# Optimization experiments

Hardware: AMD Instinct MI355X
Metric: run time of the kernel (lower is better)

## Reference

```python
import jax, jax.numpy as jnp
import numpy as np

EMBED_DIM = 1024
NUM_HEADS = 16
HEAD_DIM = EMBED_DIM // NUM_HEADS


def setup_inputs() -> dict:
    key = jax.random.key(0)
    ks = jax.random.split(key, 7)
    B, S, D = 2, 2048, EMBED_DIM
    scale = 1.0 / np.sqrt(D)
    return {
        "query": jax.random.normal(ks[0], (B, S, D), dtype=jnp.float32),
        "key": jax.random.normal(ks[1], (B, S, D), dtype=jnp.float32),
        "value": jax.random.normal(ks[2], (B, S, D), dtype=jnp.float32),
        "W_qkv": jax.random.normal(ks[3], (D, 3 * D), dtype=jnp.float32) * scale,
        "b_qkv": jnp.zeros((3 * D,), dtype=jnp.float32),
        "W_out": jax.random.normal(ks[4], (D, D), dtype=jnp.float32) * scale,
        "b_out": jnp.zeros((D,), dtype=jnp.float32),
    }


def reference(query, key, value, W_qkv, b_qkv, W_out, b_out):
    # NOTE: the original torch forward ignores `key` and `value` — q,k,v all
    # come from qkv_proj(query). We keep them as args for signature fidelity.
    B, S, D = query.shape
    H, hd = NUM_HEADS, HEAD_DIM
    scale = hd ** -0.5

    qkv = query @ W_qkv + b_qkv                      # [B, S, 3D]
    qkv = qkv.reshape(B, S, 3, H, hd)
    q = jnp.transpose(qkv[:, :, 0], (0, 2, 1, 3))    # [B, H, S, hd]
    k = jnp.transpose(qkv[:, :, 1], (0, 2, 1, 3))
    v = jnp.transpose(qkv[:, :, 2], (0, 2, 1, 3))

    scores = jnp.einsum("bhsd,bhtd->bhst", q, k) * scale  # [B, H, S, S]
    attn = jax.nn.softmax(scores, axis=-1)
    out = jnp.einsum("bhst,bhtd->bhsd", attn, v)           # [B, H, S, hd]
    out = jnp.transpose(out, (0, 2, 1, 3)).reshape(B, S, D)
    return out @ W_out + b_out
```

## Files before the change

### kernel.cpp

```cpp
#include <hip/hip_runtime.h>
#include <stdint.h>

#define DEV static __device__ __forceinline__

typedef __attribute__((ext_vector_type(4))) float f32x4;
typedef __attribute__((ext_vector_type(16))) float f32x16;
typedef __attribute__((ext_vector_type(8))) short bf16x8;
typedef bf16x8 __attribute__((may_alias)) bf16x8_a;
typedef __attribute__((ext_vector_type(2))) unsigned int u32x2;
typedef u32x2 __attribute__((may_alias)) u32x2_a;

DEV unsigned short f2bf(float f) {
  union { float f; unsigned int u; } v; v.f = f;
  return (unsigned short)((v.u + 0x7FFFu + ((v.u >> 16) & 1u)) >> 16);
}

DEV float bf2f(unsigned short s) {
  union { unsigned int u; float f; } v; v.u = ((unsigned int)s) << 16;
  return v.f;
}

DEV float fast_exp2(float x) {
  float r;
  asm("v_exp_f32 %0, %1" : "=v"(r) : "v"(x));
  return r;
}

DEV unsigned int pktrunc(float lo, float hi) {
  union { float f; unsigned int u; } a, b; a.f = lo; b.f = hi;
  return __builtin_amdgcn_perm(b.u, a.u, 0x07060302u);
}

DEV void gload_lds16(const void* g, void* l) {
  __builtin_amdgcn_global_load_lds(
      (const __attribute__((address_space(1))) unsigned int*)g,
      (__attribute__((address_space(3))) unsigned int*)l, 16, 0, 0);
}

DEV void transpose_body(const float* __restrict__ in, unsigned short* __restrict__ out,
                        int R, int C, int bx, int by, int t, float (*tile)[33]) {
  const int r = t >> 3, c4 = (t & 7) << 2;
  const int tr = by << 5, tc = bx << 5;
  const float4 v = *(const float4*)(in + (size_t)(tr + r) * C + tc + c4);
  tile[r][c4] = v.x; tile[r][c4 + 1] = v.y; tile[r][c4 + 2] = v.z; tile[r][c4 + 3] = v.w;
  __syncthreads();
  ushort4 o;
  o.x = f2bf(tile[c4][r]); o.y = f2bf(tile[c4 + 1][r]);
  o.z = f2bf(tile[c4 + 2][r]); o.w = f2bf(tile[c4 + 3][r]);
  *(ushort4*)(out + (size_t)(tc + r) * R + tr + c4) = o;
}

__global__ __launch_bounds__(256) void prep_k(const float4* __restrict__ q4,
                                              ushort4* __restrict__ Xb,
                                              const float* __restrict__ Wqkv,
                                              unsigned short* __restrict__ WqkvT,
                                              const float* __restrict__ Wout,
                                              unsigned short* __restrict__ WoutT) {
  __shared__ float tile[32][33];
  const int t = threadIdx.x, bid = blockIdx.x;
  if (bid < 4096) {
    const int i = bid * 256 + t;
    float4 f = q4[i];
    ushort4 o; o.x = f2bf(f.x); o.y = f2bf(f.y); o.z = f2bf(f.z); o.w = f2bf(f.w);
    Xb[i] = o;
  } else if (bid < 4096 + 3072) {
    const int id = bid - 4096;
    transpose_body(Wqkv, WqkvT, 1024, 3072, id % 96, id / 96, t, tile);
  } else {
    const int id = bid - 4096 - 3072;
    transpose_body(Wout, WoutT, 1024, 1024, id & 31, id >> 5, t, tile);
  }
}

template <int EPI, int BN>
__global__ __launch_bounds__(256, 3) void gemm_bt(const unsigned short* __restrict__ A,
                                                  const unsigned short* __restrict__ BT,
                                                  const float* __restrict__ bias,
                                                  float* __restrict__ Cout,
                                                  unsigned short* __restrict__ q_buf,
                                                  unsigned short* __restrict__ k_buf,
                                                  unsigned short* __restrict__ vT_buf,
                                                  int M, int N, int K) {
  constexpr int NI = BN / 32;
  constexpr int NW = BN / 2;
  __shared__ unsigned short As[128 * 64];
  __shared__ unsigned short Bs[BN * 64];
  const int t = threadIdx.x, w = t >> 6, l = t & 63;
  const int wm = w >> 1, wn = w & 1;
  const int lg = l >> 4, ln = l & 15;

  const int xcd = blockIdx.x & 7, jb = blockIdx.x >> 3;
  const int m0 = (xcd * 4 + (jb & 3)) * 128;
  const int n0 = (jb >> 2) * BN;

  const int sch = (t & 7) ^ ((t >> 3) & 7);

  f32x4 acc[4][NI] = {};

#define STAGE97(k0)                                                                      \
  do {                                                                                   \
    _Pragma("unroll")                                                                    \
    for (int j = 0; j < 4; ++j)                                                          \
      gload_lds16(A + (size_t)(m0 + (t >> 3) + j * 32) * K + (k0) + sch * 8,             \
                  &As[((t >> 3) + j * 32) * 64 + (t & 7) * 8]);                          \
    _Pragma("unroll")                                                                    \
    for (int j = 0; j < BN / 32; ++j)                                                    \
      gload_lds16(BT + (size_t)(n0 + (t >> 3) + j * 32) * K + (k0) + sch * 8,            \
                  &Bs[((t >> 3) + j * 32) * 64 + (t & 7) * 8]);                          \
  } while (0)

  for (int kt = 0; kt < K; kt += 64) {
    STAGE97(kt);
    __syncthreads();
#pragma unroll
    for (int kk = 0; kk < 2; ++kk) {
      bf16x8 af[4], bfr[NI];
#pragma unroll
      for (int mi = 0; mi < 4; ++mi)
        af[mi] = *(const bf16x8_a*)&As[(wm * 64 + mi * 16 + ln) * 64 +
                                       (((kk * 4 + lg) ^ (ln & 7)) << 3)];
#pragma unroll
      for (int ni = 0; ni < NI; ++ni)
        bfr[ni] = *(const bf16x8_a*)&Bs[(wn * NW + ni * 16 + ln) * 64 +
                                        (((kk * 4 + lg) ^ (ln & 7)) << 3)];
#pragma unroll
      for (int mi = 0; mi < 4; ++mi)
#pragma unroll
        for (int ni = 0; ni < NI; ++ni)
          acc[mi][ni] = __builtin_amdgcn_mfma_f32_16x16x32_bf16(af[mi], bfr[ni], acc[mi][ni], 0, 0, 0);
    }
    __syncthreads();
  }
#undef STAGE97

#pragma unroll
  for (int ni = 0; ni < NI; ++ni) {
    const int c = n0 + wn * NW + ni * 16 + ln;
    const float bv = bias[c];
    if (EPI == 1) {
      const int which = c >> 10;
      const int h = (c >> 6) & 15;
      const int d = c & 63;
#pragma unroll
      for (int mi = 0; mi < 4; ++mi) {
        const int mrow = m0 + wm * 64 + mi * 16 + lg * 4;
        const int b = mrow >> 11, s = mrow & 2047;
        const size_t bh = (size_t)(b * 16 + h);
        f32x4 v = acc[mi][ni];
        if (which == 0) {
          const float QSCALE = 0.125f * 1.44269504088896340736f;
          unsigned short* dst = q_buf + (bh * 2048 + s) * 64 + d;
#pragma unroll
          for (int r = 0; r < 4; ++r) dst[(size_t)r * 64] = f2bf((v[r] + bv) * QSCALE);
        } else if (which == 1) {
          unsigned short* dst = k_buf + (bh * 2048 + s) * 64 + d;
#pragma unroll
          for (int r = 0; r < 4; ++r) dst[(size_t)r * 64] = f2bf(v[r] + bv);
        } else {
          const int sp = (s & ~12) | ((s & 4) << 1) | ((s & 8) >> 1);
          unsigned short* dst = vT_buf + (bh * 64 + d) * 2048 + sp;
          ushort4 o4;
          o4.x = f2bf(v[0] + bv); o4.y = f2bf(v[1] + bv); o4.z = f2bf(v[2] + bv); o4.w = f2bf(v[3] + bv);
          *(ushort4*)dst = o4;
        }
      }
    } else {
#pragma unroll
      for (int mi = 0; mi < 4; ++mi) {
        const int mrow = m0 + wm * 64 + mi * 16 + lg * 4;
        f32x4 v = acc[mi][ni];
#pragma unroll
        for (int r = 0; r < 4; ++r) Cout[(size_t)(mrow + r) * N + c] = v[r] + bv;
      }
    }
  }
}

template <int SPLIT>
__global__ __launch_bounds__(256, 4) void attn_k(const unsigned short* __restrict__ Qb,
                                                 const unsigned short* __restrict__ Kb,
                                                 const unsigned short* __restrict__ Vt,
                                                 unsigned short* __restrict__ AO,
                                                 unsigned short* __restrict__ Opart,
                                                 float* __restrict__ lpart) {
  constexpr int NT = 32 / SPLIT;
  const float SHIFT = -16.0f;
  __shared__ unsigned short Ks[2][64 * 64];
  __shared__ unsigned short Vs[2][64 * 64];

  const int t = threadIdx.x, w = t >> 6, l = t & 63;
  const int l31 = l & 31, lh = l >> 5;
  const int xcd = blockIdx.x & 7, idx = blockIdx.x >> 3;
  const int bh = xcd * 4 + (idx & 3);
  const int qt = (SPLIT == 2) ? ((idx >> 2) & 15) : (idx >> 2);
  const int half = (SPLIT == 2) ? (idx >> 6) : 0;
  const int b = bh >> 4, h = bh & 15;
  const unsigned short* Q = Qb + (size_t)bh * 2048 * 64;
  const unsigned short* K = Kb + (size_t)bh * 2048 * 64 + (size_t)half * NT * 64 * 64;
  const unsigned short* V = Vt + (size_t)bh * 64 * 2048 + half * NT * 64;
  const int qbase = qt * 128 + w * 32;

  const int srow = t >> 3;
  const int scol = ((t & 7) ^ (srow & 7)) << 3;
  const int dcol = (t & 7) << 3;

  bf16x8 qf[4];
#pragma unroll
  for (int kd = 0; kd < 4; ++kd)
    qf[kd] = *(const bf16x8_a*)(Q + (size_t)(qbase + l31) * 64 + kd * 16 + lh * 8);

  bf16x8 ones;
#pragma unroll
  for (int i = 0; i < 8; ++i) ones[i] = (short)0x3F80;

  f32x16 o32[2] = {};
  f32x16 lsum = {};

  {
    gload_lds16(K + (size_t)srow * 64 + scol,        &Ks[0][srow * 64 + dcol]);
    gload_lds16(K + (size_t)(srow + 32) * 64 + scol, &Ks[0][(srow + 32) * 64 + dcol]);
    gload_lds16(V + (size_t)srow * 2048 + scol,        &Vs[0][srow * 64 + dcol]);
    gload_lds16(V + (size_t)(srow + 32) * 2048 + scol, &Vs[0][(srow + 32) * 64 + dcol]);
  }
  __syncthreads();

  for (int tk = 0; tk < NT; ++tk) {
    const int cur = tk & 1;
    if (tk < NT - 1) {
      const int k1 = (tk + 1) * 64;
      const unsigned short* Kg = K + (size_t)k1 * 64;
      const unsigned short* Vg = V + k1;
      gload_lds16(Kg + (size_t)srow * 64 + scol,        &Ks[cur ^ 1][srow * 64 + dcol]);
      gload_lds16(Kg + (size_t)(srow + 32) * 64 + scol, &Ks[cur ^ 1][(srow + 32) * 64 + dcol]);
      gload_lds16(Vg + (size_t)srow * 2048 + scol,        &Vs[cur ^ 1][srow * 64 + dcol]);
      gload_lds16(Vg + (size_t)(srow + 32) * 2048 + scol, &Vs[cur ^ 1][(srow + 32) * 64 + dcol]);
    }

    f32x16 sa[2] = {};
#pragma unroll
    for (int m2 = 0; m2 < 2; ++m2)
#pragma unroll
      for (int kd = 0; kd < 4; ++kd) {
        const bf16x8 kf = *(const bf16x8_a*)
            &Ks[cur][(m2 * 32 + l31) * 64 + (((kd * 2 + lh) ^ (l & 7)) << 3)];
        sa[m2] = __builtin_amdgcn_mfma_f32_32x32x16_bf16(kf, qf[kd], sa[m2], 0, 0, 0);
      }

    bf16x8 vf0[4];
#pragma unroll
    for (int ksI = 0; ksI < 4; ++ksI)
      vf0[ksI] = *(const bf16x8_a*)&Vs[cur][l31 * 64 + (((ksI * 2 + lh) ^ (l & 7)) << 3)];

    unsigned int pk[2][8];
#pragma unroll
    for (int m2 = 0; m2 < 2; ++m2) {
      float p[16];
#pragma unroll
      for (int r = 0; r < 16; ++r) p[r] = fast_exp2(sa[m2][r] + SHIFT);
#pragma unroll
      for (int u = 0; u < 8; ++u) pk[m2][u] = pktrunc(p[2 * u], p[2 * u + 1]);
    }

    union { unsigned int u[4]; bf16x8 v; } pa[4];
#pragma unroll
    for (int m2 = 0; m2 < 2; ++m2)
#pragma unroll
      for (int ks2 = 0; ks2 < 2; ++ks2) {
        const int ksI = m2 * 2 + ks2;
        pa[ksI].u[0] = pk[m2][ks2 * 4 + 0];
        pa[ksI].u[1] = pk[m2][ks2 * 4 + 1];
        pa[ksI].u[2] = pk[m2][ks2 * 4 + 2];
        pa[ksI].u[3] = pk[m2][ks2 * 4 + 3];
      }
#pragma unroll
    for (int ksI = 0; ksI < 4; ++ksI) {
      const bf16x8 vf1 = *(const bf16x8_a*)
          &Vs[cur][(32 + l31) * 64 + (((ksI * 2 + lh) ^ (l & 7)) << 3)];
      o32[0] = __builtin_amdgcn_mfma_f32_32x32x16_bf16(pa[ksI].v, vf0[ksI], o32[0], 0, 0, 0);
      lsum   = __builtin_amdgcn_mfma_f32_32x32x16_bf16(pa[ksI].v, ones,     lsum,   0, 0, 0);
      o32[1] = __builtin_amdgcn_mfma_f32_32x32x16_bf16(pa[ksI].v, vf1,      o32[1], 0, 0, 0);
    }

    __syncthreads();
  }

  if (SPLIT == 2) {
    const size_t pbase = ((size_t)(half * 32 + bh) * 2048 + qbase);
#pragma unroll
    for (int nb = 0; nb < 2; ++nb)
#pragma unroll
      for (int r = 0; r < 16; ++r) {
        const int qrow = (r & 3) + 8 * (r >> 2) + 4 * lh;
        Opart[(pbase + qrow) * 64 + nb * 32 + l31] = f2bf(o32[nb][r]);
      }
    if (l31 == 0) {
#pragma unroll
      for (int r = 0; r < 16; ++r)
        lpart[pbase + (r & 3) + 8 * (r >> 2) + 4 * lh] = lsum[r];
    }
  } else {
#pragma unroll
    for (int nb = 0; nb < 2; ++nb)
#pragma unroll
      for (int r = 0; r < 16; ++r) {
        const int qrow = (r & 3) + 8 * (r >> 2) + 4 * lh;
        const size_t row = (size_t)b * 2048 + qbase + qrow;
        AO[row * 1024 + h * 64 + nb * 32 + l31] = f2bf(o32[nb][r] / lsum[r]);
      }
  }
}

__global__ __launch_bounds__(256) void merge_k(const unsigned short* __restrict__ Opart,
                                               const float* __restrict__ lpart,
                                               unsigned short* __restrict__ AO) {
  const int u = blockIdx.x * 256 + threadIdx.x;
  const int c8 = u & 7, s = (u >> 3) & 2047, bh = u >> 14;
  const int b = bh >> 4, h = bh & 15;
  const size_t r0 = (size_t)bh * 2048 + s;
  const size_t r1 = (size_t)(32 + bh) * 2048 + s;
  const bf16x8 a0 = *(const bf16x8_a*)(Opart + r0 * 64 + c8 * 8);
  const bf16x8 a1 = *(const bf16x8_a*)(Opart + r1 * 64 + c8 * 8);
  const float inv = 1.0f / (lpart[r0] + lpart[r1]);
  bf16x8 oo;
#pragma unroll
  for (int i = 0; i < 8; ++i)
    oo[i] = (short)f2bf((bf2f((unsigned short)a0[i]) + bf2f((unsigned short)a1[i])) * inv);
  *(bf16x8_a*)(AO + ((size_t)b * 2048 + s) * 1024 + h * 64 + c8 * 8) = oo;
}

extern "C" void kernel_launch(void* const* d_in, const int* in_sizes, int n_in,
                              void* d_out, int out_size, void* d_ws, size_t ws_size,
                              hipStream_t stream) {
  const float* query = (const float*)d_in[0];
  const float* W_qkv = (const float*)d_in[3];
  const float* b_qkv = (const float*)d_in[4];
  const float* W_out = (const float*)d_in[5];
  const float* b_out = (const float*)d_in[6];
  float* out = (float*)d_out;
  char* ws = (char*)d_ws;

  unsigned short* Xb    = (unsigned short*)(ws);
  unsigned short* WqkvT = (unsigned short*)(ws + 8388608);
  unsigned short* WoutT = (unsigned short*)(ws + 14680064);
  unsigned short* qb    = (unsigned short*)(ws + 16777216);
  unsigned short* kb    = (unsigned short*)(ws + 25165824);
  unsigned short* vT    = (unsigned short*)(ws + 33554432);
  unsigned short* Opart = (unsigned short*)(ws + 41943040);
  float*          lpart = (float*)(ws + 58720256);
  const bool split2 = ws_size >= 59244544;
  unsigned short* AO    = Xb;

  prep_k<<<8192, 256, 0, stream>>>((const float4*)query, (ushort4*)Xb,
                                   W_qkv, WqkvT, W_out, WoutT);
  gemm_bt<1, 128><<<768, 256, 0, stream>>>(Xb, WqkvT, b_qkv, nullptr, qb, kb, vT,
                                           4096, 3072, 1024);
  if (split2) {
    attn_k<2><<<1024, 256, 0, stream>>>(qb, kb, vT, nullptr, Opart, lpart);
    merge_k<<<2048, 256, 0, stream>>>(Opart, lpart, AO);
  } else {
    attn_k<1><<<512, 256, 0, stream>>>(qb, kb, vT, AO, nullptr, nullptr);
  }
  gemm_bt<0, 64><<<512, 256, 0, stream>>>(AO, WoutT, b_out, out, nullptr, nullptr, nullptr,
                                          4096, 1024, 1024);
}
```

Measured before the change: 113.8 us.

## Double per-wave query rows in attention to reuse K/V fragments

Each wave now handles 64 query rows (two 32-row blocks) instead of 32, so K and V fragments loaded from LDS are reused across two QK^T and PV passes. The block's query tile grows from 128 to 256 rows and the grid is halved, with launch bounds relaxed to 2 blocks per CU to give room for the doubled accumulators. The aim is fewer LDS reads and fewer global K/V tile loads per query row. The cost is higher register pressure, lower occupancy, and fewer blocks (512 in the split path) to fill the GPU.

```diff
diff --git a/kernel.cpp b/kernel.cpp
--- a/kernel.cpp
+++ b/kernel.cpp
@@ -177,7 +177,7 @@
 }
 
 template <int SPLIT>
-__global__ __launch_bounds__(256, 4) void attn_k(const unsigned short* __restrict__ Qb,
+__global__ __launch_bounds__(256, 2) void attn_k(const unsigned short* __restrict__ Qb,
                                                  const unsigned short* __restrict__ Kb,
                                                  const unsigned short* __restrict__ Vt,
                                                  unsigned short* __restrict__ AO,
@@ -192,29 +192,32 @@
   const int l31 = l & 31, lh = l >> 5;
   const int xcd = blockIdx.x & 7, idx = blockIdx.x >> 3;
   const int bh = xcd * 4 + (idx & 3);
-  const int qt = (SPLIT == 2) ? ((idx >> 2) & 15) : (idx >> 2);
-  const int half = (SPLIT == 2) ? (idx >> 6) : 0;
+  const int rest = idx >> 2;
+  const int qt = rest & 7;
+  const int half = (SPLIT == 2) ? (rest >> 3) : 0;
   const int b = bh >> 4, h = bh & 15;
   const unsigned short* Q = Qb + (size_t)bh * 2048 * 64;
   const unsigned short* K = Kb + (size_t)bh * 2048 * 64 + (size_t)half * NT * 64 * 64;
   const unsigned short* V = Vt + (size_t)bh * 64 * 2048 + half * NT * 64;
-  const int qbase = qt * 128 + w * 32;
+  const int qbase = qt * 256 + w * 64;
 
   const int srow = t >> 3;
   const int scol = ((t & 7) ^ (srow & 7)) << 3;
   const int dcol = (t & 7) << 3;
 
-  bf16x8 qf[4];
-#pragma unroll
-  for (int kd = 0; kd < 4; ++kd)
-    qf[kd] = *(const bf16x8_a*)(Q + (size_t)(qbase + l31) * 64 + kd * 16 + lh * 8);
+  bf16x8 qf[2][4];
+#pragma unroll
+  for (int qb = 0; qb < 2; ++qb)
+#pragma unroll
+    for (int kd = 0; kd < 4; ++kd)
+      qf[qb][kd] = *(const bf16x8_a*)(Q + (size_t)(qbase + qb * 32 + l31) * 64 + kd * 16 + lh * 8);
 
   bf16x8 ones;
 #pragma unroll
   for (int i = 0; i < 8; ++i) ones[i] = (short)0x3F80;
 
-  f32x16 o32[2] = {};
-  f32x16 lsum = {};
+  f32x16 o32[2][2] = {};
+  f32x16 lsum[2] = {};
 
   {
     gload_lds16(K + (size_t)srow * 64 + scol,        &Ks[0][srow * 64 + dcol]);
@@ -236,49 +239,57 @@
       gload_lds16(Vg + (size_t)(srow + 32) * 2048 + scol, &Vs[cur ^ 1][(srow + 32) * 64 + dcol]);
     }
 
-    f32x16 sa[2] = {};
+    bf16x8 kf[2][4];
 #pragma unroll
     for (int m2 = 0; m2 < 2; ++m2)
 #pragma unroll
-      for (int kd = 0; kd < 4; ++kd) {
-        const bf16x8 kf = *(const bf16x8_a*)
-            &Ks[cur][(m2 * 32 + l31) * 64 + (((kd * 2 + lh) ^ (l & 7)) << 3)];
-        sa[m2] = __builtin_amdgcn_mfma_f32_32x32x16_bf16(kf, qf[kd], sa[m2], 0, 0, 0);
+      for (int kd = 0; kd < 4; ++kd)
+        kf[m2][kd] = *(const bf16x8_a*)
+            &Ks[cur][(m2 * 32 + l31) * 64 + (((kd * 2 + lh) ^ (l31 & 7)) << 3)];
+    bf16x8 vf[2][4];
+#pragma unroll
+    for (int nb = 0; nb < 2; ++nb)
+#pragma unroll
+      for (int ksI = 0; ksI < 4; ++ksI)
+        vf[nb][ksI] = *(const bf16x8_a*)
+            &Vs[cur][(nb * 32 + l31) * 64 + (((ksI * 2 + lh) ^ (l31 & 7)) << 3)];
+
+#pragma unroll
+    for (int qb = 0; qb < 2; ++qb) {
+      f32x16 sa[2] = {};
+#pragma unroll
+      for (int m2 = 0; m2 < 2; ++m2)
+#pragma unroll
+        for (int kd = 0; kd < 4; ++kd)
+          sa[m2] = __builtin_amdgcn_mfma_f32_32x32x16_bf16(kf[m2][kd], qf[qb][kd], sa[m2], 0, 0, 0);
+
+      unsigned int pk[2][8];
+#pragma unroll
+      for (int m2 = 0; m2 < 2; ++m2) {
+        float p[16];
+#pragma unroll
+        for (int r = 0; r < 16; ++r) p[r] = fast_exp2(sa[m2][r] + SHIFT);
+#pragma unroll
+        for (int u = 0; u < 8; ++u) pk[m2][u] = pktrunc(p[2 * u], p[2 * u + 1]);
       }
 
-    bf16x8 vf0[4];
-#pragma unroll
-    for (int ksI = 0; ksI < 4; ++ksI)
-      vf0[ksI] = *(const bf16x8_a*)&Vs[cur][l31 * 64 + (((ksI * 2 + lh) ^ (l & 7)) << 3)];
-
-    unsigned int pk[2][8];
-#pragma unroll
-    for (int m2 = 0; m2 < 2; ++m2) {
-      float p[16];
-#pragma unroll
-      for (int r = 0; r < 16; ++r) p[r] = fast_exp2(sa[m2][r] + SHIFT);
-#pragma unroll
-      for (int u = 0; u < 8; ++u) pk[m2][u] = pktrunc(p[2 * u], p[2 * u + 1]);
-    }
-
-    union { unsigned int u[4]; bf16x8 v; } pa[4];
-#pragma unroll
-    for (int m2 = 0; m2 < 2; ++m2)
-#pragma unroll
-      for (int ks2 = 0; ks2 < 2; ++ks2) {
-        const int ksI = m2 * 2 + ks2;
-        pa[ksI].u[0] = pk[m2][ks2 * 4 + 0];
-        pa[ksI].u[1] = pk[m2][ks2 * 4 + 1];
-        pa[ksI].u[2] = pk[m2][ks2 * 4 + 2];
-        pa[ksI].u[3] = pk[m2][ks2 * 4 + 3];
+      union { unsigned int u[4]; bf16x8 v; } pa[4];
+#pragma unroll
+      for (int m2 = 0; m2 < 2; ++m2)
+#pragma unroll
+        for (int ks2 = 0; ks2 < 2; ++ks2) {
+          const int ksI = m2 * 2 + ks2;
+          pa[ksI].u[0] = pk[m2][ks2 * 4 + 0];
+          pa[ksI].u[1] = pk[m2][ks2 * 4 + 1];
+          pa[ksI].u[2] = pk[m2][ks2 * 4 + 2];
+          pa[ksI].u[3] = pk[m2][ks2 * 4 + 3];
+        }
+#pragma unroll
+      for (int ksI = 0; ksI < 4; ++ksI) {
+        o32[qb][0] = __builtin_amdgcn_mfma_f32_32x32x16_bf16(pa[ksI].v, vf[0][ksI], o32[qb][0], 0, 0, 0);
+        lsum[qb]   = __builtin_amdgcn_mfma_f32_32x32x16_bf16(pa[ksI].v, ones,       lsum[qb],   0, 0, 0);
+        o32[qb][1] = __builtin_amdgcn_mfma_f32_32x32x16_bf16(pa[ksI].v, vf[1][ksI], o32[qb][1], 0, 0, 0);
       }
-#pragma unroll
-    for (int ksI = 0; ksI < 4; ++ksI) {
-      const bf16x8 vf1 = *(const bf16x8_a*)
-          &Vs[cur][(32 + l31) * 64 + (((ksI * 2 + lh) ^ (l & 7)) << 3)];
-      o32[0] = __builtin_amdgcn_mfma_f32_32x32x16_bf16(pa[ksI].v, vf0[ksI], o32[0], 0, 0, 0);
-      lsum   = __builtin_amdgcn_mfma_f32_32x32x16_bf16(pa[ksI].v, ones,     lsum,   0, 0, 0);
-      o32[1] = __builtin_amdgcn_mfma_f32_32x32x16_bf16(pa[ksI].v, vf1,      o32[1], 0, 0, 0);
     }
 
     __syncthreads();
@@ -287,26 +298,32 @@
   if (SPLIT == 2) {
     const size_t pbase = ((size_t)(half * 32 + bh) * 2048 + qbase);
 #pragma unroll
-    for (int nb = 0; nb < 2; ++nb)
-#pragma unroll
-      for (int r = 0; r < 16; ++r) {
-        const int qrow = (r & 3) + 8 * (r >> 2) + 4 * lh;
-        Opart[(pbase + qrow) * 64 + nb * 32 + l31] = f2bf(o32[nb][r]);
-      }
+    for (int qb = 0; qb < 2; ++qb)
+#pragma unroll
+      for (int nb = 0; nb < 2; ++nb)
+#pragma unroll
+        for (int r = 0; r < 16; ++r) {
+          const int qrow = (r & 3) + 8 * (r >> 2) + 4 * lh;
+          Opart[(pbase + qb * 32 + qrow) * 64 + nb * 32 + l31] = f2bf(o32[qb][nb][r]);
+        }
     if (l31 == 0) {
 #pragma unroll
-      for (int r = 0; r < 16; ++r)
-        lpart[pbase + (r & 3) + 8 * (r >> 2) + 4 * lh] = lsum[r];
+      for (int qb = 0; qb < 2; ++qb)
+#pragma unroll
+        for (int r = 0; r < 16; ++r)
+          lpart[pbase + qb * 32 + (r & 3) + 8 * (r >> 2) + 4 * lh] = lsum[qb][r];
     }
   } else {
 #pragma unroll
-    for (int nb = 0; nb < 2; ++nb)
-#pragma unroll
-      for (int r = 0; r < 16; ++r) {
-        const int qrow = (r & 3) + 8 * (r >> 2) + 4 * lh;
-        const size_t row = (size_t)b * 2048 + qbase + qrow;
-        AO[row * 1024 + h * 64 + nb * 32 + l31] = f2bf(o32[nb][r] / lsum[r]);
-      }
+    for (int qb = 0; qb < 2; ++qb)
+#pragma unroll
+      for (int nb = 0; nb < 2; ++nb)
+#pragma unroll
+        for (int r = 0; r < 16; ++r) {
+          const int qrow = (r & 3) + 8 * (r >> 2) + 4 * lh;
+          const size_t row = (size_t)b * 2048 + qbase + qb * 32 + qrow;
+          AO[row * 1024 + h * 64 + nb * 32 + l31] = f2bf(o32[qb][nb][r] / lsum[qb][r]);
+        }
   }
 }
 
@@ -355,10 +372,10 @@
   gemm_bt<1, 128><<<768, 256, 0, stream>>>(Xb, WqkvT, b_qkv, nullptr, qb, kb, vT,
                                            4096, 3072, 1024);
   if (split2) {
-    attn_k<2><<<1024, 256, 0, stream>>>(qb, kb, vT, nullptr, Opart, lpart);
+    attn_k<2><<<512, 256, 0, stream>>>(qb, kb, vT, nullptr, Opart, lpart);
     merge_k<<<2048, 256, 0, stream>>>(Opart, lpart, AO);
   } else {
-    attn_k<1><<<512, 256, 0, stream>>>(qb, kb, vT, AO, nullptr, nullptr);
+    attn_k<1><<<256, 256, 0, stream>>>(qb, kb, vT, AO, nullptr, nullptr);
   }
   gemm_bt<0, 64><<<512, 256, 0, stream>>>(AO, WoutT, b_out, out, nullptr, nullptr, nullptr,
                                           4096, 1024, 1024);
```

After: 113.6 us. About the same (-0.2%).

## Store V in MFMA fragment order and load directly from global memory

Applied to the files above, without the earlier changes.

The QKV GEMM epilogue now writes V in a pre-swizzled per-tile fragment layout, so each lane's bf16x8 operand for the PV MFMA sits contiguously. The attention kernel drops the V shared-memory double buffer and loads V fragments straight from global/L2 into registers. This removes LDS traffic and LDS footprint for V and may improve occupancy. The cost is that V loads are no longer prefetched a tile ahead, so global-memory latency can be exposed inside the loop.

```diff
diff --git a/kernel.cpp b/kernel.cpp
--- a/kernel.cpp
+++ b/kernel.cpp
@@ -79,7 +79,7 @@
                                                   float* __restrict__ Cout,
                                                   unsigned short* __restrict__ q_buf,
                                                   unsigned short* __restrict__ k_buf,
-                                                  unsigned short* __restrict__ vT_buf,
+                                                  unsigned short* __restrict__ vfrag,
                                                   int M, int N, int K) {
   constexpr int NI = BN / 32;
   constexpr int NW = BN / 2;
@@ -157,8 +157,9 @@
 #pragma unroll
           for (int r = 0; r < 4; ++r) dst[(size_t)r * 64] = f2bf(v[r] + bv);
         } else {
-          const int sp = (s & ~12) | ((s & 4) << 1) | ((s & 8) >> 1);
-          unsigned short* dst = vT_buf + (bh * 64 + d) * 2048 + sp;
+          unsigned short* dst = vfrag +
+              (((bh * 32 + (size_t)(s >> 6)) * 2 + ((d >> 5) & 1)) * 4 + ((s >> 4) & 3)) * 512 +
+              ((s >> 2) & 1) * 256 + (d & 31) * 8 + ((s >> 3) & 1) * 4;
           ushort4 o4;
           o4.x = f2bf(v[0] + bv); o4.y = f2bf(v[1] + bv); o4.z = f2bf(v[2] + bv); o4.w = f2bf(v[3] + bv);
           *(ushort4*)dst = o4;
@@ -179,14 +180,13 @@
 template <int SPLIT>
 __global__ __launch_bounds__(256, 4) void attn_k(const unsigned short* __restrict__ Qb,
                                                  const unsigned short* __restrict__ Kb,
-                                                 const unsigned short* __restrict__ Vt,
+                                                 const unsigned short* __restrict__ Vf,
                                                  unsigned short* __restrict__ AO,
                                                  unsigned short* __restrict__ Opart,
                                                  float* __restrict__ lpart) {
   constexpr int NT = 32 / SPLIT;
   const float SHIFT = -16.0f;
   __shared__ unsigned short Ks[2][64 * 64];
-  __shared__ unsigned short Vs[2][64 * 64];
 
   const int t = threadIdx.x, w = t >> 6, l = t & 63;
   const int l31 = l & 31, lh = l >> 5;
@@ -197,7 +197,7 @@
   const int b = bh >> 4, h = bh & 15;
   const unsigned short* Q = Qb + (size_t)bh * 2048 * 64;
   const unsigned short* K = Kb + (size_t)bh * 2048 * 64 + (size_t)half * NT * 64 * 64;
-  const unsigned short* V = Vt + (size_t)bh * 64 * 2048 + half * NT * 64;
+  const unsigned short* V = Vf + ((size_t)bh * 32 + half * NT) * 4096;
   const int qbase = qt * 128 + w * 32;
 
   const int srow = t >> 3;
@@ -219,21 +219,15 @@
   {
     gload_lds16(K + (size_t)srow * 64 + scol,        &Ks[0][srow * 64 + dcol]);
     gload_lds16(K + (size_t)(srow + 32) * 64 + scol, &Ks[0][(srow + 32) * 64 + dcol]);
-    gload_lds16(V + (size_t)srow * 2048 + scol,        &Vs[0][srow * 64 + dcol]);
-    gload_lds16(V + (size_t)(srow + 32) * 2048 + scol, &Vs[0][(srow + 32) * 64 + dcol]);
   }
   __syncthreads();
 
   for (int tk = 0; tk < NT; ++tk) {
     const int cur = tk & 1;
     if (tk < NT - 1) {
-      const int k1 = (tk + 1) * 64;
-      const unsigned short* Kg = K + (size_t)k1 * 64;
-      const unsigned short* Vg = V + k1;
+      const unsigned short* Kg = K + (size_t)(tk + 1) * 64 * 64;
       gload_lds16(Kg + (size_t)srow * 64 + scol,        &Ks[cur ^ 1][srow * 64 + dcol]);
       gload_lds16(Kg + (size_t)(srow + 32) * 64 + scol, &Ks[cur ^ 1][(srow + 32) * 64 + dcol]);
-      gload_lds16(Vg + (size_t)srow * 2048 + scol,        &Vs[cur ^ 1][srow * 64 + dcol]);
-      gload_lds16(Vg + (size_t)(srow + 32) * 2048 + scol, &Vs[cur ^ 1][(srow + 32) * 64 + dcol]);
     }
 
     f32x16 sa[2] = {};
@@ -246,10 +240,13 @@
         sa[m2] = __builtin_amdgcn_mfma_f32_32x32x16_bf16(kf, qf[kd], sa[m2], 0, 0, 0);
       }
 
-    bf16x8 vf0[4];
-#pragma unroll
-    for (int ksI = 0; ksI < 4; ++ksI)
-      vf0[ksI] = *(const bf16x8_a*)&Vs[cur][l31 * 64 + (((ksI * 2 + lh) ^ (l & 7)) << 3)];
+    const unsigned short* Vt_ = V + (size_t)tk * 4096;
+    bf16x8 vf[2][4];
+#pragma unroll
+    for (int nb = 0; nb < 2; ++nb)
+#pragma unroll
+      for (int ksI = 0; ksI < 4; ++ksI)
+        vf[nb][ksI] = *(const bf16x8_a*)(Vt_ + ((nb * 4 + ksI) << 9) + l * 8);
 
     unsigned int pk[2][8];
 #pragma unroll
@@ -274,11 +271,9 @@
       }
 #pragma unroll
     for (int ksI = 0; ksI < 4; ++ksI) {
-      const bf16x8 vf1 = *(const bf16x8_a*)
-          &Vs[cur][(32 + l31) * 64 + (((ksI * 2 + lh) ^ (l & 7)) << 3)];
-      o32[0] = __builtin_amdgcn_mfma_f32_32x32x16_bf16(pa[ksI].v, vf0[ksI], o32[0], 0, 0, 0);
-      lsum   = __builtin_amdgcn_mfma_f32_32x32x16_bf16(pa[ksI].v, ones,     lsum,   0, 0, 0);
-      o32[1] = __builtin_amdgcn_mfma_f32_32x32x16_bf16(pa[ksI].v, vf1,      o32[1], 0, 0, 0);
+      o32[0] = __builtin_amdgcn_mfma_f32_32x32x16_bf16(pa[ksI].v, vf[0][ksI], o32[0], 0, 0, 0);
+      lsum   = __builtin_amdgcn_mfma_f32_32x32x16_bf16(pa[ksI].v, ones,       lsum,   0, 0, 0);
+      o32[1] = __builtin_amdgcn_mfma_f32_32x32x16_bf16(pa[ksI].v, vf[1][ksI], o32[1], 0, 0, 0);
     }
 
     __syncthreads();
@@ -344,7 +339,7 @@
   unsigned short* WoutT = (unsigned short*)(ws + 14680064);
   unsigned short* qb    = (unsigned short*)(ws + 16777216);
   unsigned short* kb    = (unsigned short*)(ws + 25165824);
-  unsigned short* vT    = (unsigned short*)(ws + 33554432);
+  unsigned short* vfrag = (unsigned short*)(ws + 33554432);
   unsigned short* Opart = (unsigned short*)(ws + 41943040);
   float*          lpart = (float*)(ws + 58720256);
   const bool split2 = ws_size >= 59244544;
@@ -352,13 +347,13 @@
 
   prep_k<<<8192, 256, 0, stream>>>((const float4*)query, (ushort4*)Xb,
                                    W_qkv, WqkvT, W_out, WoutT);
-  gemm_bt<1, 128><<<768, 256, 0, stream>>>(Xb, WqkvT, b_qkv, nullptr, qb, kb, vT,
+  gemm_bt<1, 128><<<768, 256, 0, stream>>>(Xb, WqkvT, b_qkv, nullptr, qb, kb, vfrag,
                                            4096, 3072, 1024);
   if (split2) {
-    attn_k<2><<<1024, 256, 0, stream>>>(qb, kb, vT, nullptr, Opart, lpart);
+    attn_k<2><<<1024, 256, 0, stream>>>(qb, kb, vfrag, nullptr, Opart, lpart);
     merge_k<<<2048, 256, 0, stream>>>(Opart, lpart, AO);
   } else {
-    attn_k<1><<<512, 256, 0, stream>>>(qb, kb, vT, AO, nullptr, nullptr);
+    attn_k<1><<<512, 256, 0, stream>>>(qb, kb, vfrag, AO, nullptr, nullptr);
   }
   gemm_bt<0, 64><<<512, 256, 0, stream>>>(AO, WoutT, b_out, out, nullptr, nullptr, nullptr,
                                           4096, 1024, 1024);
```

Result: slower. 116.5 us (+2.3%).
